# Kernel optimization log

Hardware: AMD Instinct MI355X
Metric: run time of the kernel (lower is better)

## Reference

```python
import jax, jax.numpy as jnp
import numpy as np

N_NODES = 50000
N_EDGES = 1600000
NUM_FEATURES = 128
HIDDEN = 32
HEADS = 4
NUM_CLASSES = 32
NEG_SLOPE = 0.2


def setup_inputs() -> dict:
    key = jax.random.key(0)
    ks = jax.random.split(key, 10)
    glorot = lambda k, shp: jax.random.normal(k, shp, jnp.float32) * jnp.sqrt(2.0 / (shp[0] + shp[-1]))
    return {
        "x": jax.random.normal(ks[0], (N_NODES, NUM_FEATURES), jnp.float32),
        "edge_index": jax.random.randint(ks[1], (2, N_EDGES), 0, N_NODES, jnp.int32),
        "W1": glorot(ks[2], (NUM_FEATURES, HEADS * HIDDEN)),
        "att_src1": glorot(ks[3], (HEADS, HIDDEN)),
        "att_dst1": glorot(ks[4], (HEADS, HIDDEN)),
        "b1": jnp.zeros((HEADS * HIDDEN,), jnp.float32),
        "W2": glorot(ks[5], (HEADS * HIDDEN, NUM_CLASSES)),
        "att_src2": glorot(ks[6], (1, NUM_CLASSES)),
        "att_dst2": glorot(ks[7], (1, NUM_CLASSES)),
        "b2": jnp.zeros((NUM_CLASSES,), jnp.float32),
    }


def _leaky_relu(v):
    return jnp.where(v >= 0, v, NEG_SLOPE * v)


def _gat_conv(x, src, dst, W, att_src, att_dst, bias, heads, ch, concat):
    # x: [N, F_in]; src/dst: [E] (self-loops already included)
    n = x.shape[0]
    h = (x @ W).reshape(n, heads, ch)                    # [N, H, C]
    a_src = jnp.sum(h * att_src[None], axis=-1)          # [N, H]
    a_dst = jnp.sum(h * att_dst[None], axis=-1)          # [N, H]
    e = _leaky_relu(a_src[src] + a_dst[dst])             # [E, H]
    # segment softmax over incoming edges of each dst node
    mx = jax.ops.segment_max(e, dst, num_segments=n)     # [N, H]
    mx = jnp.where(jnp.isfinite(mx), mx, 0.0)
    mx = jax.lax.stop_gradient(mx)
    ex = jnp.exp(e - mx[dst])                            # [E, H]
    den = jax.ops.segment_sum(ex, dst, num_segments=n)   # [N, H]
    alpha = ex / (den[dst] + 1e-16)                      # [E, H]
    out = jax.ops.segment_sum(h[src] * alpha[:, :, None], dst, num_segments=n)  # [N, H, C]
    if concat:
        out = out.reshape(n, heads * ch)
    else:
        out = out.mean(axis=1)
    return out + bias


def _add_self_loops(edge_index, n):
    loops = jnp.arange(n, dtype=edge_index.dtype)
    src = jnp.concatenate([edge_index[0], loops])
    dst = jnp.concatenate([edge_index[1], loops])
    return src, dst


def reference(x, edge_index, W1, att_src1, att_dst1, b1, W2, att_src2, att_dst2, b2):
    src, dst = _add_self_loops(edge_index, x.shape[0])
    h = _gat_conv(x, src, dst, W1, att_src1, att_dst1, b1, HEADS, HIDDEN, True)
    h = jax.nn.relu(h)
    out = _gat_conv(h, src, dst, W2, att_src2, att_dst2, b2, 1, NUM_CLASSES, False)
    return jax.nn.softmax(out, axis=1)
```

## Files before the change

kernel.cpp:

```cpp
#include <hip/hip_runtime.h>
#include <math.h>

#define HEADS 4
#define HID 32
#define FEAT 128
#define NCLS 32
#define NS 0.2f
#define CHUNK 4096
#define BSTRIDE 12288

__device__ __forceinline__ unsigned short f2bf(float x) {
    unsigned u = __float_as_uint(x);
    unsigned r = (u + 0x7FFFu + ((u >> 16) & 1u)) >> 16;
    return (unsigned short)r;
}
__device__ __forceinline__ float2 bf2x2(unsigned u) {
    float2 r;
    r.x = __uint_as_float(u << 16);
    r.y = __uint_as_float(u & 0xFFFF0000u);
    return r;
}

__device__ __forceinline__ void scan256(int* arr, int tid, int* wsum) {
    int v = arr[tid];
    int incl = v;
    #pragma unroll
    for (int off = 1; off < 64; off <<= 1) {
        int t = __shfl_up(incl, off, 64);
        if ((tid & 63) >= off) incl += t;
    }
    int wid = tid >> 6;
    if ((tid & 63) == 63) wsum[wid] = incl;
    __syncthreads();
    int wpre = 0;
    #pragma unroll
    for (int w = 0; w < 3; ++w) if (w < wid) wpre += wsum[w];
    arr[tid] = wpre + incl - v;
    __syncthreads();
}

__global__ __launch_bounds__(256) void cursor_init_kernel(int* __restrict__ gcursor) {
    gcursor[threadIdx.x] = threadIdx.x * BSTRIDE;
}

__global__ __launch_bounds__(256) void bin_kernel(
    const int* __restrict__ ei, int E, int ET,
    int* __restrict__ gcursor, unsigned int* __restrict__ binned) {
    __shared__ int hist[256];
    __shared__ int lcur[256];
    __shared__ int rbase[256];
    __shared__ int wsum[4];
    __shared__ unsigned int stage[CHUNK];
    __shared__ unsigned short sbkt[CHUNK];
    int tid = threadIdx.x;
    int cb = blockIdx.x * CHUNK;
    int sv[16], dv[16];
    hist[tid] = 0;
    __syncthreads();
    #pragma unroll
    for (int r = 0; r < 16; ++r) {
        int i = cb + r * 256 + tid;
        int s = 0, d = -1;
        if (i < ET) {
            if (i < E) { s = ei[i]; d = ei[E + i]; }
            else { s = d = i - E; }
            atomicAdd(&hist[d >> 8], 1);
        }
        sv[r] = s; dv[r] = d;
    }
    __syncthreads();
    int c = hist[tid];
    rbase[tid] = c ? atomicAdd(&gcursor[tid], c) : 0;
    scan256(hist, tid, wsum);
    lcur[tid] = hist[tid];
    __syncthreads();
    #pragma unroll
    for (int r = 0; r < 16; ++r) {
        if (dv[r] >= 0) {
            int b = dv[r] >> 8;
            int slot = atomicAdd(&lcur[b], 1);
            stage[slot] = (unsigned int)sv[r] | ((unsigned int)(dv[r] & 255) << 16);
            sbkt[slot] = (unsigned short)b;
        }
    }
    __syncthreads();
    int nval = ET - cb; if (nval > CHUNK) nval = CHUNK;
    for (int j = tid; j < nval; j += 256) {
        int b = sbkt[j];
        binned[rbase[b] + (j - hist[b])] = stage[j];
    }
}

__global__ __launch_bounds__(256) void csr_kernel(
    unsigned int* __restrict__ binned, const int* __restrict__ gcursor,
    int* __restrict__ offs, int* __restrict__ oend, int N) {
    __shared__ int ncnt[256];
    __shared__ int ncur[256];
    __shared__ int wsum[4];
    __shared__ unsigned short lcsr[BSTRIDE];
    int b = blockIdx.x, tid = threadIdx.x;
    int base = b * BSTRIDE;
    int cnt = gcursor[b] - base;
    if (cnt > BSTRIDE) cnt = BSTRIDE;
    ncnt[tid] = 0;
    __syncthreads();
    for (int j = tid; j < cnt; j += 256)
        atomicAdd(&ncnt[(binned[base + j] >> 16) & 255], 1);
    __syncthreads();
    int c = ncnt[tid];
    __syncthreads();
    scan256(ncnt, tid, wsum);
    int pre = ncnt[tid];
    int g = (b << 8) + tid;
    if (g < N) { offs[g] = base + pre; oend[g] = base + pre + c; }
    ncur[tid] = pre;
    __syncthreads();
    for (int j = tid; j < cnt; j += 256) {
        unsigned int u = binned[base + j];
        int p = atomicAdd(&ncur[(u >> 16) & 255], 1);
        lcsr[p] = (unsigned short)(u & 0xFFFFu);
    }
    __syncthreads();
    for (int j = tid; j < cnt; j += 256)
        binned[base + j] = (unsigned int)lcsr[j];
}

__global__ __launch_bounds__(256) void gemm1_kernel(
    const float* __restrict__ x, const float* __restrict__ W1,
    const float* __restrict__ as1, const float* __restrict__ ad1,
    unsigned short* __restrict__ h1b, float* __restrict__ a1s,
    float* __restrict__ a1d, int N) {
    __shared__ float xs[64][32];
    __shared__ float ws[32][128];
    int tid = threadIdx.x;
    int tx = tid & 31;
    int ty = tid >> 5;
    int row0 = blockIdx.x * 64;
    float4 acc[8];
    #pragma unroll
    for (int r = 0; r < 8; ++r) acc[r] = make_float4(0.f, 0.f, 0.f, 0.f);

    for (int k0 = 0; k0 < FEAT; k0 += 32) {
        __syncthreads();
        #pragma unroll
        for (int i = tid; i < 512; i += 256) {
            int r = i >> 3, c4 = i & 7;
            int n = row0 + r;
            float4 v = (n < N) ? *(const float4*)(x + (size_t)n * FEAT + k0 + c4 * 4)
                               : make_float4(0.f, 0.f, 0.f, 0.f);
            *(float4*)&xs[r][c4 * 4] = v;
        }
        #pragma unroll
        for (int i = tid; i < 1024; i += 256) {
            int k = i >> 5, c4 = i & 31;
            *(float4*)&ws[k][c4 * 4] =
                *(const float4*)(W1 + (size_t)(k0 + k) * FEAT + c4 * 4);
        }
        __syncthreads();

        for (int k = 0; k < 32; k += 4) {
            float4 xv[8];
            #pragma unroll
            for (int r = 0; r < 8; ++r) xv[r] = *(float4*)&xs[ty * 8 + r][k];
            #pragma unroll
            for (int kk = 0; kk < 4; ++kk) {
                float4 wv = *(float4*)&ws[k + kk][tx * 4];
                #pragma unroll
                for (int r = 0; r < 8; ++r) {
                    float xr = (kk == 0) ? xv[r].x : (kk == 1) ? xv[r].y
                             : (kk == 2) ? xv[r].z : xv[r].w;
                    acc[r].x += xr * wv.x;
                    acc[r].y += xr * wv.y;
                    acc[r].z += xr * wv.z;
                    acc[r].w += xr * wv.w;
                }
            }
        }
    }
    int hd = tx >> 3;
    float4 av = *(const float4*)(as1 + tx * 4);
    float4 dv = *(const float4*)(ad1 + tx * 4);
    #pragma unroll
    for (int r = 0; r < 8; ++r) {
        int n = row0 + ty * 8 + r;
        if (n >= N) break;
        unsigned int lo = (unsigned)f2bf(acc[r].x) | ((unsigned)f2bf(acc[r].y) << 16);
        unsigned int hi = (unsigned)f2bf(acc[r].z) | ((unsigned)f2bf(acc[r].w) << 16);
        uint2 pk; pk.x = lo; pk.y = hi;
        *(uint2*)(h1b + (size_t)n * FEAT + tx * 4) = pk;
        float vs = acc[r].x * av.x + acc[r].y * av.y + acc[r].z * av.z + acc[r].w * av.w;
        float vd = acc[r].x * dv.x + acc[r].y * dv.y + acc[r].z * dv.z + acc[r].w * dv.w;
        #pragma unroll
        for (int off = 4; off; off >>= 1) {
            vs += __shfl_down(vs, off);
            vd += __shfl_down(vd, off);
        }
        if ((tx & 7) == 0) {
            a1s[n * HEADS + hd] = vs;
            a1d[n * HEADS + hd] = vd;
        }
    }
}

__global__ __launch_bounds__(256) void agg1_kernel(
    const unsigned short* __restrict__ h1b, const float* __restrict__ a1s,
    const float* __restrict__ a1d, const int* __restrict__ offs,
    const int* __restrict__ oend, const int* __restrict__ csr,
    const float* __restrict__ b1, float* __restrict__ hout, int N) {
    __shared__ float exs[4][64][4];
    __shared__ int   sN[4][64];
    int wv = threadIdx.x >> 6;
    int d = blockIdx.x * 4 + wv;
    bool active = (d < N);
    int lane = threadIdx.x & 63;
    int beg = 0, end = 0, deg = 0;
    float4 adv = make_float4(0.f, 0.f, 0.f, 0.f);
    if (active) {
        beg = offs[d]; end = oend[d]; deg = end - beg;
        adv = *(const float4*)(a1d + d * 4);
    }

    float al0 = 0.f, al1 = 0.f, al2 = 0.f, al3 = 0.f;
    int s_e = 0;
    if (active && lane < deg && deg <= 64) {
        s_e = csr[beg + lane];
        float4 as = *(const float4*)(a1s + s_e * 4);
        float e0 = as.x + adv.x; e0 = e0 >= 0.f ? e0 : NS * e0; al0 = __expf(e0);
        float e1 = as.y + adv.y; e1 = e1 >= 0.f ? e1 : NS * e1; al1 = __expf(e1);
        float e2 = as.z + adv.z; e2 = e2 >= 0.f ? e2 : NS * e2; al2 = __expf(e2);
        float e3 = as.w + adv.w; e3 = e3 >= 0.f ? e3 : NS * e3; al3 = __expf(e3);
    }
    sN[wv][lane] = s_e;
    *(float4*)&exs[wv][lane][0] = make_float4(al0, al1, al2, al3);
    __syncthreads();
    if (!active) return;

    int q = lane >> 4, sub = lane & 15;
    int cl = sub * 8;
    int h3 = sub >> 2;
    float2 c0 = {0.f, 0.f}, c1 = {0.f, 0.f}, c2 = {0.f, 0.f}, c3 = {0.f, 0.f};
    float inv;

    if (deg <= 64) {
        float dn0 = al0, dn1 = al1, dn2 = al2, dn3 = al3;
        #pragma unroll
        for (int off = 32; off; off >>= 1) {
            dn0 += __shfl_xor(dn0, off);
            dn1 += __shfl_xor(dn1, off);
            dn2 += __shfl_xor(dn2, off);
            dn3 += __shfl_xor(dn3, off);
        }
        float dnh = (h3 == 0) ? dn0 : (h3 == 1) ? dn1 : (h3 == 2) ? dn2 : dn3;
        inv = 1.0f / (dnh + 1e-16f);
        for (int e = q; e < deg; e += 16) {
            int e1i = e + 4, e2i = e + 8, e3i = e + 12;
            int s0 = sN[wv][e],   s1 = sN[wv][e1i];
            int s2 = sN[wv][e2i], s3 = sN[wv][e3i];
            float a0 = exs[wv][e][h3],   a1 = exs[wv][e1i][h3];
            float a2 = exs[wv][e2i][h3], a3 = exs[wv][e3i][h3];
            uint4 A = *(const uint4*)(h1b + (size_t)s0 * FEAT + cl);
            uint4 B = *(const uint4*)(h1b + (size_t)s1 * FEAT + cl);
            uint4 C = *(const uint4*)(h1b + (size_t)s2 * FEAT + cl);
            uint4 D = *(const uint4*)(h1b + (size_t)s3 * FEAT + cl);
            float2 t;
            t = bf2x2(A.x); c0.x += t.x * a0; c0.y += t.y * a0;
            t = bf2x2(A.y); c1.x += t.x * a0; c1.y += t.y * a0;
            t = bf2x2(A.z); c2.x += t.x * a0; c2.y += t.y * a0;
            t = bf2x2(A.w); c3.x += t.x * a0; c3.y += t.y * a0;
            t = bf2x2(B.x); c0.x += t.x * a1; c0.y += t.y * a1;
            t = bf2x2(B.y); c1.x += t.x * a1; c1.y += t.y * a1;
            t = bf2x2(B.z); c2.x += t.x * a1; c2.y += t.y * a1;
            t = bf2x2(B.w); c3.x += t.x * a1; c3.y += t.y * a1;
            t = bf2x2(C.x); c0.x += t.x * a2; c0.y += t.y * a2;
            t = bf2x2(C.y); c1.x += t.x * a2; c1.y += t.y * a2;
            t = bf2x2(C.z); c2.x += t.x * a2; c2.y += t.y * a2;
            t = bf2x2(C.w); c3.x += t.x * a2; c3.y += t.y * a2;
            t = bf2x2(D.x); c0.x += t.x * a3; c0.y += t.y * a3;
            t = bf2x2(D.y); c1.x += t.x * a3; c1.y += t.y * a3;
            t = bf2x2(D.z); c2.x += t.x * a3; c2.y += t.y * a3;
            t = bf2x2(D.w); c3.x += t.x * a3; c3.y += t.y * a3;
        }
    } else {
        float adh = (h3 == 0) ? adv.x : (h3 == 1) ? adv.y : (h3 == 2) ? adv.z : adv.w;
        float dn = 0.f;
        for (int i = beg; i < end; i += 16) {
            int i0 = i + q, i1 = i + 4 + q, i2 = i + 8 + q, i3 = i + 12 + q;
            bool v0 = i0 < end, v1 = i1 < end, v2 = i2 < end, v3 = i3 < end;
            int s0 = csr[v0 ? i0 : beg];
            int s1 = csr[v1 ? i1 : beg];
            int s2 = csr[v2 ? i2 : beg];
            int s3 = csr[v3 ? i3 : beg];
            float e0 = a1s[s0 * 4 + h3] + adh; e0 = e0 >= 0.f ? e0 : NS * e0;
            float e1 = a1s[s1 * 4 + h3] + adh; e1 = e1 >= 0.f ? e1 : NS * e1;
            float e2 = a1s[s2 * 4 + h3] + adh; e2 = e2 >= 0.f ? e2 : NS * e2;
            float e3 = a1s[s3 * 4 + h3] + adh; e3 = e3 >= 0.f ? e3 : NS * e3;
            float al0f = v0 ? __expf(e0) : 0.f;
            float al1f = v1 ? __expf(e1) : 0.f;
            float al2f = v2 ? __expf(e2) : 0.f;
            float al3f = v3 ? __expf(e3) : 0.f;
            dn += (al0f + al1f) + (al2f + al3f);
            uint4 A = *(const uint4*)(h1b + (size_t)s0 * FEAT + cl);
            uint4 B = *(const uint4*)(h1b + (size_t)s1 * FEAT + cl);
            uint4 C = *(const uint4*)(h1b + (size_t)s2 * FEAT + cl);
            uint4 D = *(const uint4*)(h1b + (size_t)s3 * FEAT + cl);
            float2 t;
            t = bf2x2(A.x); c0.x += t.x * al0f; c0.y += t.y * al0f;
            t = bf2x2(A.y); c1.x += t.x * al0f; c1.y += t.y * al0f;
            t = bf2x2(A.z); c2.x += t.x * al0f; c2.y += t.y * al0f;
            t = bf2x2(A.w); c3.x += t.x * al0f; c3.y += t.y * al0f;
            t = bf2x2(B.x); c0.x += t.x * al1f; c0.y += t.y * al1f;
            t = bf2x2(B.y); c1.x += t.x * al1f; c1.y += t.y * al1f;
            t = bf2x2(B.z); c2.x += t.x * al1f; c2.y += t.y * al1f;
            t = bf2x2(B.w); c3.x += t.x * al1f; c3.y += t.y * al1f;
            t = bf2x2(C.x); c0.x += t.x * al2f; c0.y += t.y * al2f;
            t = bf2x2(C.y); c1.x += t.x * al2f; c1.y += t.y * al2f;
            t = bf2x2(C.z); c2.x += t.x * al2f; c2.y += t.y * al2f;
            t = bf2x2(C.w); c3.x += t.x * al2f; c3.y += t.y * al2f;
            t = bf2x2(D.x); c0.x += t.x * al3f; c0.y += t.y * al3f;
            t = bf2x2(D.y); c1.x += t.x * al3f; c1.y += t.y * al3f;
            t = bf2x2(D.z); c2.x += t.x * al3f; c2.y += t.y * al3f;
            t = bf2x2(D.w); c3.x += t.x * al3f; c3.y += t.y * al3f;
        }
        dn += __shfl_xor(dn, 16);
        dn += __shfl_xor(dn, 32);
        inv = 1.0f / (dn + 1e-16f);
    }
    #pragma unroll
    for (int off = 32; off >= 16; off >>= 1) {
        c0.x += __shfl_xor(c0.x, off); c0.y += __shfl_xor(c0.y, off);
        c1.x += __shfl_xor(c1.x, off); c1.y += __shfl_xor(c1.y, off);
        c2.x += __shfl_xor(c2.x, off); c2.y += __shfl_xor(c2.y, off);
        c3.x += __shfl_xor(c3.x, off); c3.y += __shfl_xor(c3.y, off);
    }
    if (q == 0) {
        float4 b0 = *(const float4*)(b1 + cl);
        float4 b4 = *(const float4*)(b1 + cl + 4);
        float4 o0, o1;
        o0.x = c0.x * inv + b0.x; o0.x = o0.x > 0.f ? o0.x : 0.f;
        o0.y = c0.y * inv + b0.y; o0.y = o0.y > 0.f ? o0.y : 0.f;
        o0.z = c1.x * inv + b0.z; o0.z = o0.z > 0.f ? o0.z : 0.f;
        o0.w = c1.y * inv + b0.w; o0.w = o0.w > 0.f ? o0.w : 0.f;
        o1.x = c2.x * inv + b4.x; o1.x = o1.x > 0.f ? o1.x : 0.f;
        o1.y = c2.y * inv + b4.y; o1.y = o1.y > 0.f ? o1.y : 0.f;
        o1.z = c3.x * inv + b4.z; o1.z = o1.z > 0.f ? o1.z : 0.f;
        o1.w = c3.y * inv + b4.w; o1.w = o1.w > 0.f ? o1.w : 0.f;
        *(float4*)(hout + (size_t)d * FEAT + cl) = o0;
        *(float4*)(hout + (size_t)d * FEAT + cl + 4) = o1;
    }
}

__global__ __launch_bounds__(256) void gemm2_kernel(
    const float* __restrict__ h, const float* __restrict__ W2,
    const float* __restrict__ as2, const float* __restrict__ ad2,
    unsigned short* __restrict__ g2b, float* __restrict__ a2s,
    float* __restrict__ a2d, int N) {
    __shared__ float xs[128][33];
    __shared__ float ws[FEAT][NCLS];
    int tid = threadIdx.x;
    int tx = tid & 7;
    int ty = tid >> 3;
    int row0 = blockIdx.x * 128;

    #pragma unroll
    for (int i = tid; i < FEAT * NCLS / 4; i += 256) {
        int k = i >> 3, c4 = i & 7;
        *(float4*)&ws[k][c4 * 4] = *(const float4*)(W2 + (size_t)k * NCLS + c4 * 4);
    }

    float4 acc[4];
    #pragma unroll
    for (int r = 0; r < 4; ++r) acc[r] = make_float4(0.f, 0.f, 0.f, 0.f);

    for (int k0 = 0; k0 < FEAT; k0 += 32) {
        __syncthreads();
        #pragma unroll
        for (int i = tid; i < 1024; i += 256) {
            int r = i >> 3, c4 = i & 7;
            int n = row0 + r;
            float4 v = (n < N) ? *(const float4*)(h + (size_t)n * FEAT + k0 + c4 * 4)
                               : make_float4(0.f, 0.f, 0.f, 0.f);
            xs[r][c4 * 4 + 0] = v.x;
            xs[r][c4 * 4 + 1] = v.y;
            xs[r][c4 * 4 + 2] = v.z;
            xs[r][c4 * 4 + 3] = v.w;
        }
        __syncthreads();

        for (int k = 0; k < 32; k += 4) {
            #pragma unroll
            for (int kk = 0; kk < 4; ++kk) {
                float4 wv = *(float4*)&ws[k0 + k + kk][tx * 4];
                #pragma unroll
                for (int r = 0; r < 4; ++r) {
                    float xr = xs[ty * 4 + r][k + kk];
                    acc[r].x += xr * wv.x;
                    acc[r].y += xr * wv.y;
                    acc[r].z += xr * wv.z;
                    acc[r].w += xr * wv.w;
                }
            }
        }
    }
    float4 av = *(const float4*)(as2 + tx * 4);
    float4 dv = *(const float4*)(ad2 + tx * 4);
    #pragma unroll
    for (int r = 0; r < 4; ++r) {
        int n = row0 + ty * 4 + r;
        if (n >= N) break;
        unsigned int lo = (unsigned)f2bf(acc[r].x) | ((unsigned)f2bf(acc[r].y) << 16);
        unsigned int hi = (unsigned)f2bf(acc[r].z) | ((unsigned)f2bf(acc[r].w) << 16);
        uint2 pk; pk.x = lo; pk.y = hi;
        *(uint2*)(g2b + (size_t)n * NCLS + tx * 4) = pk;
        float vs = acc[r].x * av.x + acc[r].y * av.y + acc[r].z * av.z + acc[r].w * av.w;
        float vd = acc[r].x * dv.x + acc[r].y * dv.y + acc[r].z * dv.z + acc[r].w * dv.w;
        #pragma unroll
        for (int off = 4; off; off >>= 1) {
            vs += __shfl_down(vs, off);
            vd += __shfl_down(vd, off);
        }
        if (tx == 0) { a2s[n] = vs; a2d[n] = vd; }
    }
}

__global__ __launch_bounds__(256) void agg2_kernel(
    const unsigned short* __restrict__ g2b, const float* __restrict__ a2s,
    const float* __restrict__ a2d, const int* __restrict__ offs,
    const int* __restrict__ oend, const int* __restrict__ csr,
    const float* __restrict__ b2, float* __restrict__ out, int N) {
    int d = blockIdx.x * 4 + (threadIdx.x >> 6);
    if (d >= N) return;
    int lane = threadIdx.x & 63;
    int beg = offs[d], end = oend[d];
    float ad = a2d[d];

    int q = lane >> 4, sub = lane & 15;
    int ch2 = sub * 2;
    float dn = 0.f;
    float2 ac = {0.f, 0.f};
    for (int i = beg; i < end; i += 16) {
        int i0 = i + q, i1 = i + 4 + q, i2 = i + 8 + q, i3 = i + 12 + q;
        bool v0 = i0 < end, v1 = i1 < end, v2 = i2 < end, v3 = i3 < end;
        int s0 = csr[v0 ? i0 : beg];
        int s1 = csr[v1 ? i1 : beg];
        int s2 = csr[v2 ? i2 : beg];
        int s3 = csr[v3 ? i3 : beg];
        float e0 = a2s[s0] + ad; e0 = e0 >= 0.f ? e0 : NS * e0;
        float e1 = a2s[s1] + ad; e1 = e1 >= 0.f ? e1 : NS * e1;
        float e2 = a2s[s2] + ad; e2 = e2 >= 0.f ? e2 : NS * e2;
        float e3 = a2s[s3] + ad; e3 = e3 >= 0.f ? e3 : NS * e3;
        float al0 = v0 ? __expf(e0) : 0.f;
        float al1 = v1 ? __expf(e1) : 0.f;
        float al2 = v2 ? __expf(e2) : 0.f;
        float al3 = v3 ? __expf(e3) : 0.f;
        dn += (al0 + al1) + (al2 + al3);
        unsigned int A = *(const unsigned int*)(g2b + (size_t)s0 * NCLS + ch2);
        unsigned int B = *(const unsigned int*)(g2b + (size_t)s1 * NCLS + ch2);
        unsigned int C = *(const unsigned int*)(g2b + (size_t)s2 * NCLS + ch2);
        unsigned int D = *(const unsigned int*)(g2b + (size_t)s3 * NCLS + ch2);
        float2 t;
        t = bf2x2(A); ac.x += t.x * al0; ac.y += t.y * al0;
        t = bf2x2(B); ac.x += t.x * al1; ac.y += t.y * al1;
        t = bf2x2(C); ac.x += t.x * al2; ac.y += t.y * al2;
        t = bf2x2(D); ac.x += t.x * al3; ac.y += t.y * al3;
    }
    dn += __shfl_xor(dn, 16);
    dn += __shfl_xor(dn, 32);
    #pragma unroll
    for (int off = 32; off >= 16; off >>= 1) {
        ac.x += __shfl_xor(ac.x, off);
        ac.y += __shfl_xor(ac.y, off);
    }
    float inv = 1.0f / (dn + 1e-16f);
    float2 bb = *(const float2*)(b2 + ch2);
    float v0 = ac.x * inv + bb.x;
    float v1 = ac.y * inv + bb.y;
    float m = fmaxf(v0, v1);
    #pragma unroll
    for (int off = 8; off; off >>= 1) m = fmaxf(m, __shfl_xor(m, off, 16));
    float e0 = __expf(v0 - m), e1 = __expf(v1 - m);
    float sm = e0 + e1;
    #pragma unroll
    for (int off = 8; off; off >>= 1) sm += __shfl_xor(sm, off, 16);
    if (q == 0) {
        float2 o; o.x = e0 / sm; o.y = e1 / sm;
        *(float2*)(out + (size_t)d * NCLS + ch2) = o;
    }
}

extern "C" void kernel_launch(void* const* d_in, const int* in_sizes, int n_in,
                              void* d_out, int out_size, void* d_ws, size_t ws_size,
                              hipStream_t stream) {
    const float* x   = (const float*)d_in[0];
    const int*   ei  = (const int*)d_in[1];
    const float* W1  = (const float*)d_in[2];
    const float* as1 = (const float*)d_in[3];
    const float* ad1 = (const float*)d_in[4];
    const float* b1  = (const float*)d_in[5];
    const float* W2  = (const float*)d_in[6];
    const float* as2 = (const float*)d_in[7];
    const float* ad2 = (const float*)d_in[8];
    const float* b2  = (const float*)d_in[9];
    float* out = (float*)d_out;

    int N = in_sizes[0] / FEAT;
    int E = in_sizes[1] / 2;
    int ET = E + N;
    int NB = (N + 255) >> 8;

    float* ws   = (float*)d_ws;
    unsigned short* h1b = (unsigned short*)ws;
    float* hout = (float*)(h1b + (size_t)N * FEAT);
    unsigned short* g2b = (unsigned short*)(hout + (size_t)N * FEAT);
    float* a1s  = (float*)(g2b + (size_t)N * NCLS);
    float* a1d  = a1s + (size_t)N * HEADS;
    float* a2s  = a1d + (size_t)N * HEADS;
    float* a2d  = a2s + N;
    int* offs   = (int*)(a2d + N);
    int* oend   = offs + N;
    unsigned int* binned = (unsigned int*)(oend + N);
    int* gcursor = (int*)(binned + (size_t)256 * BSTRIDE);

    int nchunks = (ET + CHUNK - 1) / CHUNK;

    cursor_init_kernel<<<1, 256, 0, stream>>>(gcursor);
    bin_kernel<<<nchunks, 256, 0, stream>>>(ei, E, ET, gcursor, binned);
    gemm1_kernel<<<(N + 63) / 64, 256, 0, stream>>>(x, W1, as1, ad1, h1b, a1s, a1d, N);
    csr_kernel<<<NB, 256, 0, stream>>>(binned, gcursor, offs, oend, N);

    const int* csr = (const int*)binned;
    agg1_kernel<<<(N + 3) / 4, 256, 0, stream>>>(h1b, a1s, a1d, offs, oend, csr, b1, hout, N);
    gemm2_kernel<<<(N + 127) / 128, 256, 0, stream>>>(hout, W2, as2, ad2, g2b, a2s, a2d, N);
    agg2_kernel<<<(N + 3) / 4, 256, 0, stream>>>(g2b, a2s, a2d, offs, oend, csr, b2, out, N);
}
```

Measured before the change: 261.4 us.

## Fuse layer-2 linear transform and attention logits into agg1 kernel

Removes the separate gemm2 kernel and the fp32 hout intermediate. Each agg1 block now stages a transposed W2 in shared memory, writes its relu'd aggregated rows to shared memory, and computes the 32-class projection, the bf16 g2b output and the a2s/a2d logits per node. This saves a kernel launch and a full N x 128 fp32 write and re-read through global memory. In exchange, every one of the roughly 12.5k blocks reloads and transposes the 16 KB W2 and uses about 19 KB more shared memory, which may reduce occupancy of the gather-bound kernel. The transpose writes are also strided and may cause LDS bank conflicts.

```diff
diff --git a/kernel.cpp b/kernel.cpp
--- a/kernel.cpp
+++ b/kernel.cpp
@@ -206,13 +206,30 @@
     const unsigned short* __restrict__ h1b, const float* __restrict__ a1s,
     const float* __restrict__ a1d, const int* __restrict__ offs,
     const int* __restrict__ oend, const int* __restrict__ csr,
-    const float* __restrict__ b1, float* __restrict__ hout, int N) {
+    const float* __restrict__ b1, const float* __restrict__ W2,
+    const float* __restrict__ as2, const float* __restrict__ ad2,
+    unsigned short* __restrict__ g2b, float* __restrict__ a2s,
+    float* __restrict__ a2d, int N) {
+    __shared__ float W2t[NCLS][FEAT + 1];
+    __shared__ float asd[2][NCLS];
     __shared__ float exs[4][64][4];
     __shared__ int   sN[4][64];
-    int wv = threadIdx.x >> 6;
+    __shared__ float hrow[4][FEAT];
+    int tid = threadIdx.x;
+    for (int i = tid; i < FEAT * NCLS / 4; i += 256) {
+        int k = i >> 3, c4 = (i & 7) * 4;
+        float4 v = *(const float4*)(W2 + (size_t)k * NCLS + c4);
+        W2t[c4 + 0][k] = v.x;
+        W2t[c4 + 1][k] = v.y;
+        W2t[c4 + 2][k] = v.z;
+        W2t[c4 + 3][k] = v.w;
+    }
+    if (tid < NCLS) { asd[0][tid] = as2[tid]; asd[1][tid] = ad2[tid]; }
+
+    int wv = tid >> 6;
+    int lane = tid & 63;
     int d = blockIdx.x * 4 + wv;
     bool active = (d < N);
-    int lane = threadIdx.x & 63;
     int beg = 0, end = 0, deg = 0;
     float4 adv = make_float4(0.f, 0.f, 0.f, 0.f);
     if (active) {
@@ -233,97 +250,98 @@
     sN[wv][lane] = s_e;
     *(float4*)&exs[wv][lane][0] = make_float4(al0, al1, al2, al3);
     __syncthreads();
-    if (!active) return;
 
     int q = lane >> 4, sub = lane & 15;
     int cl = sub * 8;
     int h3 = sub >> 2;
     float2 c0 = {0.f, 0.f}, c1 = {0.f, 0.f}, c2 = {0.f, 0.f}, c3 = {0.f, 0.f};
-    float inv;
-
-    if (deg <= 64) {
-        float dn0 = al0, dn1 = al1, dn2 = al2, dn3 = al3;
-        #pragma unroll
-        for (int off = 32; off; off >>= 1) {
-            dn0 += __shfl_xor(dn0, off);
-            dn1 += __shfl_xor(dn1, off);
-            dn2 += __shfl_xor(dn2, off);
-            dn3 += __shfl_xor(dn3, off);
-        }
-        float dnh = (h3 == 0) ? dn0 : (h3 == 1) ? dn1 : (h3 == 2) ? dn2 : dn3;
-        inv = 1.0f / (dnh + 1e-16f);
-        for (int e = q; e < deg; e += 16) {
-            int e1i = e + 4, e2i = e + 8, e3i = e + 12;
-            int s0 = sN[wv][e],   s1 = sN[wv][e1i];
-            int s2 = sN[wv][e2i], s3 = sN[wv][e3i];
-            float a0 = exs[wv][e][h3],   a1 = exs[wv][e1i][h3];
-            float a2 = exs[wv][e2i][h3], a3 = exs[wv][e3i][h3];
-            uint4 A = *(const uint4*)(h1b + (size_t)s0 * FEAT + cl);
-            uint4 B = *(const uint4*)(h1b + (size_t)s1 * FEAT + cl);
-            uint4 C = *(const uint4*)(h1b + (size_t)s2 * FEAT + cl);
-            uint4 D = *(const uint4*)(h1b + (size_t)s3 * FEAT + cl);
-            float2 t;
-            t = bf2x2(A.x); c0.x += t.x * a0; c0.y += t.y * a0;
-            t = bf2x2(A.y); c1.x += t.x * a0; c1.y += t.y * a0;
-            t = bf2x2(A.z); c2.x += t.x * a0; c2.y += t.y * a0;
-            t = bf2x2(A.w); c3.x += t.x * a0; c3.y += t.y * a0;
-            t = bf2x2(B.x); c0.x += t.x * a1; c0.y += t.y * a1;
-            t = bf2x2(B.y); c1.x += t.x * a1; c1.y += t.y * a1;
-            t = bf2x2(B.z); c2.x += t.x * a1; c2.y += t.y * a1;
-            t = bf2x2(B.w); c3.x += t.x * a1; c3.y += t.y * a1;
-            t = bf2x2(C.x); c0.x += t.x * a2; c0.y += t.y * a2;
-            t = bf2x2(C.y); c1.x += t.x * a2; c1.y += t.y * a2;
-            t = bf2x2(C.z); c2.x += t.x * a2; c2.y += t.y * a2;
-            t = bf2x2(C.w); c3.x += t.x * a2; c3.y += t.y * a2;
-            t = bf2x2(D.x); c0.x += t.x * a3; c0.y += t.y * a3;
-            t = bf2x2(D.y); c1.x += t.x * a3; c1.y += t.y * a3;
-            t = bf2x2(D.z); c2.x += t.x * a3; c2.y += t.y * a3;
-            t = bf2x2(D.w); c3.x += t.x * a3; c3.y += t.y * a3;
-        }
-    } else {
-        float adh = (h3 == 0) ? adv.x : (h3 == 1) ? adv.y : (h3 == 2) ? adv.z : adv.w;
-        float dn = 0.f;
-        for (int i = beg; i < end; i += 16) {
-            int i0 = i + q, i1 = i + 4 + q, i2 = i + 8 + q, i3 = i + 12 + q;
-            bool v0 = i0 < end, v1 = i1 < end, v2 = i2 < end, v3 = i3 < end;
-            int s0 = csr[v0 ? i0 : beg];
-            int s1 = csr[v1 ? i1 : beg];
-            int s2 = csr[v2 ? i2 : beg];
-            int s3 = csr[v3 ? i3 : beg];
-            float e0 = a1s[s0 * 4 + h3] + adh; e0 = e0 >= 0.f ? e0 : NS * e0;
-            float e1 = a1s[s1 * 4 + h3] + adh; e1 = e1 >= 0.f ? e1 : NS * e1;
-            float e2 = a1s[s2 * 4 + h3] + adh; e2 = e2 >= 0.f ? e2 : NS * e2;
-            float e3 = a1s[s3 * 4 + h3] + adh; e3 = e3 >= 0.f ? e3 : NS * e3;
-            float al0f = v0 ? __expf(e0) : 0.f;
-            float al1f = v1 ? __expf(e1) : 0.f;
-            float al2f = v2 ? __expf(e2) : 0.f;
-            float al3f = v3 ? __expf(e3) : 0.f;
-            dn += (al0f + al1f) + (al2f + al3f);
-            uint4 A = *(const uint4*)(h1b + (size_t)s0 * FEAT + cl);
-            uint4 B = *(const uint4*)(h1b + (size_t)s1 * FEAT + cl);
-            uint4 C = *(const uint4*)(h1b + (size_t)s2 * FEAT + cl);
-            uint4 D = *(const uint4*)(h1b + (size_t)s3 * FEAT + cl);
-            float2 t;
-            t = bf2x2(A.x); c0.x += t.x * al0f; c0.y += t.y * al0f;
-            t = bf2x2(A.y); c1.x += t.x * al0f; c1.y += t.y * al0f;
-            t = bf2x2(A.z); c2.x += t.x * al0f; c2.y += t.y * al0f;
-            t = bf2x2(A.w); c3.x += t.x * al0f; c3.y += t.y * al0f;
-            t = bf2x2(B.x); c0.x += t.x * al1f; c0.y += t.y * al1f;
-            t = bf2x2(B.y); c1.x += t.x * al1f; c1.y += t.y * al1f;
-            t = bf2x2(B.z); c2.x += t.x * al1f; c2.y += t.y * al1f;
-            t = bf2x2(B.w); c3.x += t.x * al1f; c3.y += t.y * al1f;
-            t = bf2x2(C.x); c0.x += t.x * al2f; c0.y += t.y * al2f;
-            t = bf2x2(C.y); c1.x += t.x * al2f; c1.y += t.y * al2f;
-            t = bf2x2(C.z); c2.x += t.x * al2f; c2.y += t.y * al2f;
-            t = bf2x2(C.w); c3.x += t.x * al2f; c3.y += t.y * al2f;
-            t = bf2x2(D.x); c0.x += t.x * al3f; c0.y += t.y * al3f;
-            t = bf2x2(D.y); c1.x += t.x * al3f; c1.y += t.y * al3f;
-            t = bf2x2(D.z); c2.x += t.x * al3f; c2.y += t.y * al3f;
-            t = bf2x2(D.w); c3.x += t.x * al3f; c3.y += t.y * al3f;
-        }
-        dn += __shfl_xor(dn, 16);
-        dn += __shfl_xor(dn, 32);
-        inv = 1.0f / (dn + 1e-16f);
+    float inv = 0.f;
+
+    if (active) {
+        if (deg <= 64) {
+            float dn0 = al0, dn1 = al1, dn2 = al2, dn3 = al3;
+            #pragma unroll
+            for (int off = 32; off; off >>= 1) {
+                dn0 += __shfl_xor(dn0, off);
+                dn1 += __shfl_xor(dn1, off);
+                dn2 += __shfl_xor(dn2, off);
+                dn3 += __shfl_xor(dn3, off);
+            }
+            float dnh = (h3 == 0) ? dn0 : (h3 == 1) ? dn1 : (h3 == 2) ? dn2 : dn3;
+            inv = 1.0f / (dnh + 1e-16f);
+            for (int e = q; e < deg; e += 16) {
+                int e1i = e + 4, e2i = e + 8, e3i = e + 12;
+                int s0 = sN[wv][e],   s1 = sN[wv][e1i];
+                int s2 = sN[wv][e2i], s3 = sN[wv][e3i];
+                float a0 = exs[wv][e][h3],   a1 = exs[wv][e1i][h3];
+                float a2 = exs[wv][e2i][h3], a3 = exs[wv][e3i][h3];
+                uint4 A = *(const uint4*)(h1b + (size_t)s0 * FEAT + cl);
+                uint4 B = *(const uint4*)(h1b + (size_t)s1 * FEAT + cl);
+                uint4 C = *(const uint4*)(h1b + (size_t)s2 * FEAT + cl);
+                uint4 D = *(const uint4*)(h1b + (size_t)s3 * FEAT + cl);
+                float2 t;
+                t = bf2x2(A.x); c0.x += t.x * a0; c0.y += t.y * a0;
+                t = bf2x2(A.y); c1.x += t.x * a0; c1.y += t.y * a0;
+                t = bf2x2(A.z); c2.x += t.x * a0; c2.y += t.y * a0;
+                t = bf2x2(A.w); c3.x += t.x * a0; c3.y += t.y * a0;
+                t = bf2x2(B.x); c0.x += t.x * a1; c0.y += t.y * a1;
+                t = bf2x2(B.y); c1.x += t.x * a1; c1.y += t.y * a1;
+                t = bf2x2(B.z); c2.x += t.x * a1; c2.y += t.y * a1;
+                t = bf2x2(B.w); c3.x += t.x * a1; c3.y += t.y * a1;
+                t = bf2x2(C.x); c0.x += t.x * a2; c0.y += t.y * a2;
+                t = bf2x2(C.y); c1.x += t.x * a2; c1.y += t.y * a2;
+                t = bf2x2(C.z); c2.x += t.x * a2; c2.y += t.y * a2;
+                t = bf2x2(C.w); c3.x += t.x * a2; c3.y += t.y * a2;
+                t = bf2x2(D.x); c0.x += t.x * a3; c0.y += t.y * a3;
+                t = bf2x2(D.y); c1.x += t.x * a3; c1.y += t.y * a3;
+                t = bf2x2(D.z); c2.x += t.x * a3; c2.y += t.y * a3;
+                t = bf2x2(D.w); c3.x += t.x * a3; c3.y += t.y * a3;
+            }
+        } else {
+            float adh = (h3 == 0) ? adv.x : (h3 == 1) ? adv.y : (h3 == 2) ? adv.z : adv.w;
+            float dn = 0.f;
+            for (int i = beg; i < end; i += 16) {
+                int i0 = i + q, i1 = i + 4 + q, i2 = i + 8 + q, i3 = i + 12 + q;
+                bool v0 = i0 < end, v1 = i1 < end, v2 = i2 < end, v3 = i3 < end;
+                int s0 = csr[v0 ? i0 : beg];
+                int s1 = csr[v1 ? i1 : beg];
+                int s2 = csr[v2 ? i2 : beg];
+                int s3 = csr[v3 ? i3 : beg];
+                float e0 = a1s[s0 * 4 + h3] + adh; e0 = e0 >= 0.f ? e0 : NS * e0;
+                float e1 = a1s[s1 * 4 + h3] + adh; e1 = e1 >= 0.f ? e1 : NS * e1;
+                float e2 = a1s[s2 * 4 + h3] + adh; e2 = e2 >= 0.f ? e2 : NS * e2;
+                float e3 = a1s[s3 * 4 + h3] + adh; e3 = e3 >= 0.f ? e3 : NS * e3;
+                float f0 = v0 ? __expf(e0) : 0.f;
+                float f1 = v1 ? __expf(e1) : 0.f;
+                float f2 = v2 ? __expf(e2) : 0.f;
+                float f3 = v3 ? __expf(e3) : 0.f;
+                dn += (f0 + f1) + (f2 + f3);
+                uint4 A = *(const uint4*)(h1b + (size_t)s0 * FEAT + cl);
+                uint4 B = *(const uint4*)(h1b + (size_t)s1 * FEAT + cl);
+                uint4 C = *(const uint4*)(h1b + (size_t)s2 * FEAT + cl);
+                uint4 D = *(const uint4*)(h1b + (size_t)s3 * FEAT + cl);
+                float2 t;
+                t = bf2x2(A.x); c0.x += t.x * f0; c0.y += t.y * f0;
+                t = bf2x2(A.y); c1.x += t.x * f0; c1.y += t.y * f0;
+                t = bf2x2(A.z); c2.x += t.x * f0; c2.y += t.y * f0;
+                t = bf2x2(A.w); c3.x += t.x * f0; c3.y += t.y * f0;
+                t = bf2x2(B.x); c0.x += t.x * f1; c0.y += t.y * f1;
+                t = bf2x2(B.y); c1.x += t.x * f1; c1.y += t.y * f1;
+                t = bf2x2(B.z); c2.x += t.x * f1; c2.y += t.y * f1;
+                t = bf2x2(B.w); c3.x += t.x * f1; c3.y += t.y * f1;
+                t = bf2x2(C.x); c0.x += t.x * f2; c0.y += t.y * f2;
+                t = bf2x2(C.y); c1.x += t.x * f2; c1.y += t.y * f2;
+                t = bf2x2(C.z); c2.x += t.x * f2; c2.y += t.y * f2;
+                t = bf2x2(C.w); c3.x += t.x * f2; c3.y += t.y * f2;
+                t = bf2x2(D.x); c0.x += t.x * f3; c0.y += t.y * f3;
+                t = bf2x2(D.y); c1.x += t.x * f3; c1.y += t.y * f3;
+                t = bf2x2(D.z); c2.x += t.x * f3; c2.y += t.y * f3;
+                t = bf2x2(D.w); c3.x += t.x * f3; c3.y += t.y * f3;
+            }
+            dn += __shfl_xor(dn, 16);
+            dn += __shfl_xor(dn, 32);
+            inv = 1.0f / (dn + 1e-16f);
+        }
     }
     #pragma unroll
     for (int off = 32; off >= 16; off >>= 1) {
@@ -332,7 +350,7 @@
         c2.x += __shfl_xor(c2.x, off); c2.y += __shfl_xor(c2.y, off);
         c3.x += __shfl_xor(c3.x, off); c3.y += __shfl_xor(c3.y, off);
     }
-    if (q == 0) {
+    if (active && q == 0) {
         float4 b0 = *(const float4*)(b1 + cl);
         float4 b4 = *(const float4*)(b1 + cl + 4);
         float4 o0, o1;
@@ -344,81 +362,38 @@
         o1.y = c2.y * inv + b4.y; o1.y = o1.y > 0.f ? o1.y : 0.f;
         o1.z = c3.x * inv + b4.z; o1.z = o1.z > 0.f ? o1.z : 0.f;
         o1.w = c3.y * inv + b4.w; o1.w = o1.w > 0.f ? o1.w : 0.f;
-        *(float4*)(hout + (size_t)d * FEAT + cl) = o0;
-        *(float4*)(hout + (size_t)d * FEAT + cl + 4) = o1;
-    }
-}
-
-__global__ __launch_bounds__(256) void gemm2_kernel(
-    const float* __restrict__ h, const float* __restrict__ W2,
-    const float* __restrict__ as2, const float* __restrict__ ad2,
-    unsigned short* __restrict__ g2b, float* __restrict__ a2s,
-    float* __restrict__ a2d, int N) {
-    __shared__ float xs[128][33];
-    __shared__ float ws[FEAT][NCLS];
-    int tid = threadIdx.x;
-    int tx = tid & 7;
-    int ty = tid >> 3;
-    int row0 = blockIdx.x * 128;
-
-    #pragma unroll
-    for (int i = tid; i < FEAT * NCLS / 4; i += 256) {
-        int k = i >> 3, c4 = i & 7;
-        *(float4*)&ws[k][c4 * 4] = *(const float4*)(W2 + (size_t)k * NCLS + c4 * 4);
-    }
-
-    float4 acc[4];
-    #pragma unroll
-    for (int r = 0; r < 4; ++r) acc[r] = make_float4(0.f, 0.f, 0.f, 0.f);
-
-    for (int k0 = 0; k0 < FEAT; k0 += 32) {
-        __syncthreads();
+        *(float4*)&hrow[wv][cl] = o0;
+        *(float4*)&hrow[wv][cl + 4] = o1;
+    }
+    __syncthreads();
+
+    int c = lane & 31, half = lane >> 5;
+    float g = 0.f;
+    if (active) {
+        const float* hr = &hrow[wv][half * 64];
+        const float* wr = &W2t[c][half * 64];
         #pragma unroll
-        for (int i = tid; i < 1024; i += 256) {
-            int r = i >> 3, c4 = i & 7;
-            int n = row0 + r;
-            float4 v = (n < N) ? *(const float4*)(h + (size_t)n * FEAT + k0 + c4 * 4)
-                               : make_float4(0.f, 0.f, 0.f, 0.f);
-            xs[r][c4 * 4 + 0] = v.x;
-            xs[r][c4 * 4 + 1] = v.y;
-            xs[r][c4 * 4 + 2] = v.z;
-            xs[r][c4 * 4 + 3] = v.w;
-        }
-        __syncthreads();
-
-        for (int k = 0; k < 32; k += 4) {
-            #pragma unroll
-            for (int kk = 0; kk < 4; ++kk) {
-                float4 wv = *(float4*)&ws[k0 + k + kk][tx * 4];
-                #pragma unroll
-                for (int r = 0; r < 4; ++r) {
-                    float xr = xs[ty * 4 + r][k + kk];
-                    acc[r].x += xr * wv.x;
-                    acc[r].y += xr * wv.y;
-                    acc[r].z += xr * wv.z;
-                    acc[r].w += xr * wv.w;
-                }
-            }
-        }
-    }
-    float4 av = *(const float4*)(as2 + tx * 4);
-    float4 dv = *(const float4*)(ad2 + tx * 4);
-    #pragma unroll
-    for (int r = 0; r < 4; ++r) {
-        int n = row0 + ty * 4 + r;
-        if (n >= N) break;
-        unsigned int lo = (unsigned)f2bf(acc[r].x) | ((unsigned)f2bf(acc[r].y) << 16);
-        unsigned int hi = (unsigned)f2bf(acc[r].z) | ((unsigned)f2bf(acc[r].w) << 16);
-        uint2 pk; pk.x = lo; pk.y = hi;
-        *(uint2*)(g2b + (size_t)n * NCLS + tx * 4) = pk;
-        float vs = acc[r].x * av.x + acc[r].y * av.y + acc[r].z * av.z + acc[r].w * av.w;
-        float vd = acc[r].x * dv.x + acc[r].y * dv.y + acc[r].z * dv.z + acc[r].w * dv.w;
-        #pragma unroll
-        for (int off = 4; off; off >>= 1) {
-            vs += __shfl_down(vs, off);
-            vd += __shfl_down(vd, off);
-        }
-        if (tx == 0) { a2s[n] = vs; a2d[n] = vd; }
+        for (int t = 0; t < 64; t += 4) {
+            float4 hh = *(const float4*)(hr + t);
+            float4 ww = *(const float4*)(wr + t);
+            g += hh.x * ww.x + hh.y * ww.y + hh.z * ww.z + hh.w * ww.w;
+        }
+    }
+    g += __shfl_xor(g, 32);
+    float vs = g * asd[0][c];
+    float vd = g * asd[1][c];
+    #pragma unroll
+    for (int off = 1; off <= 16; off <<= 1) {
+        vs += __shfl_xor(vs, off);
+        vd += __shfl_xor(vd, off);
+    }
+    float gn = __shfl_down(g, 1);
+    if (active) {
+        if (lane == 0) { a2s[d] = vs; a2d[d] = vd; }
+        if (half == 0 && !(c & 1)) {
+            unsigned u = (unsigned)f2bf(g) | ((unsigned)f2bf(gn) << 16);
+            *(unsigned*)(g2b + (size_t)d * NCLS + c) = u;
+        }
     }
 }
 
@@ -509,8 +484,7 @@
 
     float* ws   = (float*)d_ws;
     unsigned short* h1b = (unsigned short*)ws;
-    float* hout = (float*)(h1b + (size_t)N * FEAT);
-    unsigned short* g2b = (unsigned short*)(hout + (size_t)N * FEAT);
+    unsigned short* g2b = h1b + (size_t)N * FEAT;
     float* a1s  = (float*)(g2b + (size_t)N * NCLS);
     float* a1d  = a1s + (size_t)N * HEADS;
     float* a2s  = a1d + (size_t)N * HEADS;
@@ -528,7 +502,7 @@
     csr_kernel<<<NB, 256, 0, stream>>>(binned, gcursor, offs, oend, N);
 
     const int* csr = (const int*)binned;
-    agg1_kernel<<<(N + 3) / 4, 256, 0, stream>>>(h1b, a1s, a1d, offs, oend, csr, b1, hout, N);
-    gemm2_kernel<<<(N + 127) / 128, 256, 0, stream>>>(hout, W2, as2, ad2, g2b, a2s, a2d, N);
+    agg1_kernel<<<(N + 3) / 4, 256, 0, stream>>>(h1b, a1s, a1d, offs, oend, csr,
+                                                 b1, W2, as2, ad2, g2b, a2s, a2d, N);
     agg2_kernel<<<(N + 3) / 4, 256, 0, stream>>>(g2b, a2s, a2d, offs, oend, csr, b2, out, N);
 }
```

New measurement: 335.0 us. 1.28x slower.
